# Performance work log

Hardware: AMD Instinct MI355X
Metric: run time of the kernel (lower is better)

## Reference

```python
import jax, jax.numpy as jnp
import numpy as np

B, IN_F, OUT_F = 16384, 2048, 8192


def setup_inputs() -> dict:
    key = jax.random.key(0)
    kx, kw, kb = jax.random.split(key, 3)
    bound = 1.0 / np.sqrt(IN_F)
    x = jax.random.normal(kx, (B, IN_F), dtype=jnp.float32)
    # nn.Linear default init: U(-1/sqrt(in), 1/sqrt(in)); W is (out, in)
    W = jax.random.uniform(kw, (OUT_F, IN_F), dtype=jnp.float32, minval=-bound, maxval=bound)
    b = jax.random.uniform(kb, (OUT_F,), dtype=jnp.float32, minval=-bound, maxval=bound)
    return {"x": x, "W": W, "b": b}


def reference(x, W, b):
    # Linear: (B, in) @ (in, out) + (out,) -> (B, out)
    y = jnp.einsum("bi,oi->bo", x, W) + b
    # Fused full-row sum reduction -> (B, 1)
    return jnp.sum(y, axis=-1, keepdims=True)
```

## Files before the change

### kernel.cpp

```cpp
#include <hip/hip_runtime.h>


#define B_ROWS 16384
#define IN_F   2048
#define OUT_F  8192


__global__ __launch_bounds__(256) void colsum_kernel(const float* __restrict__ W,
                                                     float* __restrict__ ws) {
    constexpr int ROWS_PER_CHUNK = 32;
    constexpr int F4_PER_ROW = IN_F / 4;
    const int h     = blockIdx.x & 1;
    const int chunk = blockIdx.x >> 1;
    const int t     = threadIdx.x;
    const int col4  = h * 256 + t;

    const float4* W4 = reinterpret_cast<const float4*>(W);
    long base = (long)(chunk * ROWS_PER_CHUNK) * F4_PER_ROW + col4;

    float4 acc = make_float4(0.f, 0.f, 0.f, 0.f);
#pragma unroll
    for (int r = 0; r < ROWS_PER_CHUNK; ++r) {
        float4 v = W4[base + (long)r * F4_PER_ROW];
        acc.x += v.x; acc.y += v.y; acc.z += v.z; acc.w += v.w;
    }
    atomicAdd(&ws[col4 * 4 + 0], acc.x);
    atomicAdd(&ws[col4 * 4 + 1], acc.y);
    atomicAdd(&ws[col4 * 4 + 2], acc.z);
    atomicAdd(&ws[col4 * 4 + 3], acc.w);
}

__global__ __launch_bounds__(256) void bsum_kernel(const float* __restrict__ b,
                                                   float* __restrict__ ws) {
    __shared__ float red[4];
    const int t = threadIdx.x;
    float acc = 0.f;
    for (int i = t; i < OUT_F; i += 256) acc += b[i];
#pragma unroll
    for (int off = 32; off > 0; off >>= 1) acc += __shfl_down(acc, off);
    if ((t & 63) == 0) red[t >> 6] = acc;
    __syncthreads();
    if (t == 0) ws[IN_F] = red[0] + red[1] + red[2] + red[3];
}

__global__ __launch_bounds__(256) void gemv_kernel(const float* __restrict__ x,
                                                   const float* __restrict__ ws,
                                                   float* __restrict__ out) {
    const int wave = threadIdx.x >> 6;
    const int lane = threadIdx.x & 63;
    const int row  = blockIdx.x * 4 + wave;

    const float4* x4 = reinterpret_cast<const float4*>(x + (long)row * IN_F);
    const float4* c4 = reinterpret_cast<const float4*>(ws);

    float acc = 0.f;
#pragma unroll
    for (int it = 0; it < IN_F / 4 / 64; ++it) {
        const int idx = it * 64 + lane;
        float4 xv = x4[idx];
        float4 cv = c4[idx];
        acc += xv.x * cv.x + xv.y * cv.y + xv.z * cv.z + xv.w * cv.w;
    }
#pragma unroll
    for (int off = 32; off > 0; off >>= 1) acc += __shfl_down(acc, off);
    if (lane == 0) out[row] = acc + ws[IN_F];
}

extern "C" void kernel_launch(void* const* d_in, const int* in_sizes, int n_in,
                              void* d_out, int out_size, void* d_ws, size_t ws_size,
                              hipStream_t stream) {
    const float* x = (const float*)d_in[0];
    const float* W = (const float*)d_in[1];
    const float* b = (const float*)d_in[2];
    float* out = (float*)d_out;
    float* ws  = (float*)d_ws;

    hipMemsetAsync(ws, 0, (IN_F + 1) * sizeof(float), stream);

    colsum_kernel<<<2 * (OUT_F / 32), 256, 0, stream>>>(W, ws);
    bsum_kernel<<<1, 256, 0, stream>>>(b, ws);
    gemv_kernel<<<B_ROWS / 4, 256, 0, stream>>>(x, ws, out);
}
```

Measured before the change: 268.7 us.

## Replace atomic column-sum accumulation with partial buffers and a deterministic reduce

The W column-sum step now writes per-chunk partial sums to a workspace buffer instead of issuing atomicAdds into a shared vector. A new reduce kernel sums the 256 partials for each column and also computes the bias sum, which removes the memset and one launch. This avoids atomic contention and makes the result deterministic. In exchange it writes and rereads a 2 MB partial buffer, and the reduce kernel runs only 9 blocks, each doing a serial 256-step loop.

```diff
diff --git a/kernel.cpp b/kernel.cpp
--- a/kernel.cpp
+++ b/kernel.cpp
@@ -5,18 +5,20 @@
 #define IN_F   2048
 #define OUT_F  8192
 
+constexpr int ROWS_PER_CHUNK = 32;
+constexpr int N_CHUNKS   = OUT_F / ROWS_PER_CHUNK;
+constexpr int F4_PER_ROW = IN_F / 4;
 
-__global__ __launch_bounds__(256) void colsum_kernel(const float* __restrict__ W,
-                                                     float* __restrict__ ws) {
-    constexpr int ROWS_PER_CHUNK = 32;
-    constexpr int F4_PER_ROW = IN_F / 4;
+constexpr int WS_P = N_CHUNKS * IN_F;
+
+__global__ __launch_bounds__(256) void colsum_partial(const float* __restrict__ W,
+                                                      float* __restrict__ ws) {
     const int h     = blockIdx.x & 1;
     const int chunk = blockIdx.x >> 1;
-    const int t     = threadIdx.x;
-    const int col4  = h * 256 + t;
+    const int col4  = h * 256 + threadIdx.x;
 
     const float4* W4 = reinterpret_cast<const float4*>(W);
-    long base = (long)(chunk * ROWS_PER_CHUNK) * F4_PER_ROW + col4;
+    long base = (long)chunk * ROWS_PER_CHUNK * F4_PER_ROW + col4;
 
     float4 acc = make_float4(0.f, 0.f, 0.f, 0.f);
 #pragma unroll
@@ -24,23 +26,26 @@
         float4 v = W4[base + (long)r * F4_PER_ROW];
         acc.x += v.x; acc.y += v.y; acc.z += v.z; acc.w += v.w;
     }
-    atomicAdd(&ws[col4 * 4 + 0], acc.x);
-    atomicAdd(&ws[col4 * 4 + 1], acc.y);
-    atomicAdd(&ws[col4 * 4 + 2], acc.z);
-    atomicAdd(&ws[col4 * 4 + 3], acc.w);
+    reinterpret_cast<float4*>(ws)[(long)chunk * F4_PER_ROW + col4] = acc;
 }
 
-__global__ __launch_bounds__(256) void bsum_kernel(const float* __restrict__ b,
-                                                   float* __restrict__ ws) {
-    __shared__ float red[4];
-    const int t = threadIdx.x;
+__global__ __launch_bounds__(256) void reduce_kernel(const float* __restrict__ b,
+                                                     float* __restrict__ ws) {
+    if (blockIdx.x == IN_F / 256) {
+        __shared__ float red[4];
+        float acc = 0.f;
+        for (int i = threadIdx.x; i < OUT_F; i += 256) acc += b[i];
+#pragma unroll
+        for (int off = 32; off > 0; off >>= 1) acc += __shfl_down(acc, off);
+        if ((threadIdx.x & 63) == 0) red[threadIdx.x >> 6] = acc;
+        __syncthreads();
+        if (threadIdx.x == 0) ws[WS_P + IN_F] = red[0] + red[1] + red[2] + red[3];
+        return;
+    }
+    const int col = blockIdx.x * 256 + threadIdx.x;
     float acc = 0.f;
-    for (int i = t; i < OUT_F; i += 256) acc += b[i];
-#pragma unroll
-    for (int off = 32; off > 0; off >>= 1) acc += __shfl_down(acc, off);
-    if ((t & 63) == 0) red[t >> 6] = acc;
-    __syncthreads();
-    if (t == 0) ws[IN_F] = red[0] + red[1] + red[2] + red[3];
+    for (int c = 0; c < N_CHUNKS; ++c) acc += ws[(long)c * IN_F + col];
+    ws[WS_P + col] = acc;
 }
 
 __global__ __launch_bounds__(256) void gemv_kernel(const float* __restrict__ x,
@@ -51,7 +56,7 @@
     const int row  = blockIdx.x * 4 + wave;
 
     const float4* x4 = reinterpret_cast<const float4*>(x + (long)row * IN_F);
-    const float4* c4 = reinterpret_cast<const float4*>(ws);
+    const float4* c4 = reinterpret_cast<const float4*>(ws + WS_P);
 
     float acc = 0.f;
 #pragma unroll
@@ -63,7 +68,7 @@
     }
 #pragma unroll
     for (int off = 32; off > 0; off >>= 1) acc += __shfl_down(acc, off);
-    if (lane == 0) out[row] = acc + ws[IN_F];
+    if (lane == 0) out[row] = acc + ws[WS_P + IN_F];
 }
 
 extern "C" void kernel_launch(void* const* d_in, const int* in_sizes, int n_in,
@@ -75,9 +80,7 @@
     float* out = (float*)d_out;
     float* ws  = (float*)d_ws;
 
-    hipMemsetAsync(ws, 0, (IN_F + 1) * sizeof(float), stream);
-
-    colsum_kernel<<<2 * (OUT_F / 32), 256, 0, stream>>>(W, ws);
-    bsum_kernel<<<1, 256, 0, stream>>>(b, ws);
+    colsum_partial<<<2 * N_CHUNKS, 256, 0, stream>>>(W, ws);
+    reduce_kernel<<<IN_F / 256 + 1, 256, 0, stream>>>(b, ws);
     gemv_kernel<<<B_ROWS / 4, 256, 0, stream>>>(x, ws, out);
 }
```

Result: faster. 246.3 us (-8.3%).
